# Kernel optimization log

Measured on AMD Instinct MI355X. Metric: run time of the kernel, lower is better.

Reference implementation:

```python
import jax, jax.numpy as jnp
import numpy as np

NUM_HEADS = 8
EMBED_CH = 512   # k channels
OUT_CH = 256     # v channels
MASK_CURRENT = False
NEG_INF = -1e30


def setup_inputs() -> dict:
    key = jax.random.key(0)
    ks = jax.random.split(key, 7)
    N, C, H, W = 8, 256, 32, 32
    s = lambda fan: 1.0 / np.sqrt(fan)
    return {
        "x": jax.random.normal(ks[0], (N, C, H, W), jnp.float32),
        "Wq": jax.random.normal(ks[1], (EMBED_CH, C), jnp.float32) * s(C),
        "bq": jax.random.normal(ks[2], (EMBED_CH,), jnp.float32) * 0.01,
        "Wkv": jax.random.normal(ks[3], (EMBED_CH + OUT_CH, C), jnp.float32) * s(C),
        "bkv": jax.random.normal(ks[4], (EMBED_CH + OUT_CH,), jnp.float32) * 0.01,
        "Wo": jax.random.normal(ks[5], (OUT_CH, OUT_CH), jnp.float32) * s(OUT_CH),
        "bo": jax.random.normal(ks[6], (OUT_CH,), jnp.float32) * 0.01,
    }


def _to_multihead(t, n, T):
    # t: [n, h*d, T] with channel layout '(h d)' -> [n, h, T, d]
    h = NUM_HEADS
    return t.reshape(n, h, -1, T).transpose(0, 1, 3, 2)


def reference(x, Wq, bq, Wkv, bkv, Wo, bo):
    n, C, H, W = x.shape
    T = H * W
    xf = x.reshape(n, C, T)  # flatten spatial dims into sequence

    # 1x1 convs == pointwise channel GEMMs
    q = jnp.einsum('oc,nct->not', Wq, xf) + bq[None, :, None]
    kv = jnp.einsum('oc,nct->not', Wkv, xf) + bkv[None, :, None]
    k, v = kv[:, :EMBED_CH], kv[:, EMBED_CH:]

    q = _to_multihead(q, n, T)   # [n, h, T, dk]
    k = _to_multihead(k, n, T)   # [n, h, T, dk]
    v = _to_multihead(v, n, T)   # [n, h, T, dv]

    dk = k.shape[-1]
    scale = 1.0 / np.sqrt(dk).astype(np.float32)

    # causal mask over flattened spatial positions (lower-triangular)
    diag = -1 if MASK_CURRENT else 0
    mask = jnp.tril(jnp.ones((T, T), dtype=bool), k=diag)  # [T, T]

    attn = jnp.einsum('nhtd,nhsd->nhts', q, k) * scale
    attn = jnp.where(mask[None, None], attn, NEG_INF)
    attn = jax.nn.softmax(attn, axis=-1)
    attn = jnp.where(mask[None, None], attn, 0.0)

    out = jnp.einsum('nhts,nhsd->nhtd', attn, v)            # [n, h, T, dv]
    out = out.transpose(0, 1, 3, 2).reshape(n, OUT_CH, T)   # n (h d) t

    out = jnp.einsum('oc,nct->not', Wo, out) + bo[None, :, None]
    return out.reshape(n, OUT_CH, H, W)
```

## Files before the change

kernel.cpp:

```cpp
#include <hip/hip_runtime.h>
#include <hip/hip_bf16.h>
#include <math.h>

typedef __bf16 bf16;
typedef __attribute__((ext_vector_type(4))) __bf16 bf16x4;
typedef __attribute__((ext_vector_type(8))) __bf16 bf16x8;
typedef __attribute__((ext_vector_type(4))) float f32x4;

#define T_DIM 1024
#define C_DIM 256
#define HEADS 8

static __device__ __forceinline__ int tb(int row, int col) {
  return row * 128 + ((((col >> 3) ^ row) & 7) << 4) + ((col & 7) << 1);
}

static __device__ __forceinline__ void gl16(const char* g, char* l) {
  __builtin_amdgcn_global_load_lds(
      (const __attribute__((address_space(1))) unsigned int*)g,
      (__attribute__((address_space(3))) unsigned int*)l, 16, 0, 0);
}
static __device__ __forceinline__ void stage16k(const char* g, char* l, int tid) {
  const int w = (tid >> 6) * 1024, ln = (tid & 63) * 16;
#pragma unroll
  for (int i = 0; i < 4; ++i) gl16(g + i * 4096 + w + ln, l + i * 4096 + w);
}
static __device__ __forceinline__ void stage8k(const char* g, char* l, int tid) {
  const int w = (tid >> 6) * 1024, ln = (tid & 63) * 16;
#pragma unroll
  for (int i = 0; i < 2; ++i) gl16(g + i * 4096 + w + ln, l + i * 4096 + w);
}
static __device__ __forceinline__ void stage4k(const char* g, char* l, int tid) {
  gl16(g + (tid >> 6) * 1024 + (tid & 63) * 16, l + (tid >> 6) * 1024);
}

__global__ __launch_bounds__(256) void k_prep(const float* __restrict__ x,
    const float* __restrict__ Wq, const float* __restrict__ Wkv, const float* __restrict__ Wo,
    char* __restrict__ xTt, char* __restrict__ Wbt, char* __restrict__ Wot) {
  const int tid = threadIdx.x;
  const int b = blockIdx.x;
  if (b < 512) {
    __shared__ float tile[64][65];
    const int n = b >> 6, rem = b & 63, tt64 = rem >> 2, ct = (rem & 3) << 6;
    const float* xp = x + ((size_t)n * C_DIM + ct) * T_DIM + tt64 * 64;
    const int t4 = (tid & 15) * 4, c0 = tid >> 4;
#pragma unroll
    for (int i = 0; i < 4; ++i) {
      const int c = c0 + i * 16;
      float4 v = *(const float4*)(xp + (size_t)c * T_DIM + t4);
      tile[c][t4] = v.x; tile[c][t4 + 1] = v.y; tile[c][t4 + 2] = v.z; tile[c][t4 + 3] = v.w;
    }
    __syncthreads();
    char* dst = xTt + (((size_t)(n * 8 + (tt64 >> 1))) * 4 + (rem & 3)) * 16384;
    const int rbase = (tt64 & 1) * 64;
#pragma unroll
    for (int i = 0; i < 2; ++i) {
      const int idx = tid + i * 256;
      const int tl = idx >> 3, c8 = (idx & 7) * 8;
      bf16x8 v;
#pragma unroll
      for (int j = 0; j < 8; ++j) v[j] = (bf16)tile[c8 + j][tl];
      *(bf16x8*)(dst + tb(rbase + tl, c8)) = v;
    }
  } else {
    const bool isWo = (b >= 532);
    const int o0 = (b - (isWo ? 532 : 512)) * 64;
#pragma unroll
    for (int i = 0; i < 8; ++i) {
      const int idx = tid + i * 256;
      const int row = idx >> 5, c8 = (idx & 31) * 8;
      const int o = o0 + row;
      const float* src = isWo ? (Wo + (size_t)o * C_DIM + c8)
                              : (o < 512 ? Wq + (size_t)o * C_DIM + c8
                                         : Wkv + (size_t)(o - 512) * C_DIM + c8);
      float4 a = *(const float4*)src;
      float4 bq4 = *(const float4*)(src + 4);
      bf16x8 v;
      v[0]=(bf16)a.x; v[1]=(bf16)a.y; v[2]=(bf16)a.z; v[3]=(bf16)a.w;
      v[4]=(bf16)bq4.x; v[5]=(bf16)bq4.y; v[6]=(bf16)bq4.z; v[7]=(bf16)bq4.w;
      char* base = isWo ? Wot : Wbt;
      char* dst = base + (((size_t)(o >> 7)) * 4 + (c8 >> 6)) * 16384;
      *(bf16x8*)(dst + tb(o & 127, c8 & 63)) = v;
    }
  }
}

__global__ __launch_bounds__(256) void k_qkv(const char* __restrict__ Wbt, const char* __restrict__ xTt,
    const float* __restrict__ bq, const float* __restrict__ bkv,
    bf16* __restrict__ q_ws, char* __restrict__ Kt, char* __restrict__ Vt) {
  __shared__ __attribute__((aligned(128))) unsigned char smem[34816];
  const int tid = threadIdx.x;
  const int nt = blockIdx.x, mt = blockIdx.y, n = blockIdx.z;
  const int w = tid >> 6, lane = tid & 63, lrow = lane & 15, lg = lane >> 4;
  const int wm = (w >> 1) * 64, wn = (w & 1) * 64;
  const char* gA = Wbt + (size_t)mt * 65536;
  const char* gB = xTt + ((size_t)(n * 8 + nt)) * 65536;
  const float s2 = 0.18033688f;

  f32x4 acc[4][4] = {};
#pragma unroll 1
  for (int kk = 0; kk < 4; ++kk) {
    stage16k(gA + kk * 16384, (char*)smem, tid);
    stage16k(gB + kk * 16384, (char*)smem + 16384, tid);
    __syncthreads();
    const char* As = (const char*)smem;
    const char* Bs = As + 16384;
    bf16x8 af[4][2], bv[4][2];
#pragma unroll
    for (int mi = 0; mi < 4; ++mi)
#pragma unroll
      for (int kh = 0; kh < 2; ++kh)
        af[mi][kh] = *(const bf16x8*)(As + tb(wm + mi * 16 + lrow, kh * 32 + lg * 8));
#pragma unroll
    for (int ni = 0; ni < 4; ++ni)
#pragma unroll
      for (int kh = 0; kh < 2; ++kh)
        bv[ni][kh] = *(const bf16x8*)(Bs + tb(wn + ni * 16 + lrow, kh * 32 + lg * 8));
#pragma unroll
    for (int kh = 0; kh < 2; ++kh)
#pragma unroll
      for (int mi = 0; mi < 4; ++mi)
#pragma unroll
        for (int ni = 0; ni < 4; ++ni)
          acc[mi][ni] = __builtin_amdgcn_mfma_f32_16x16x32_bf16(af[mi][kh], bv[ni][kh], acc[mi][ni], 0, 0, 0);
    __syncthreads();
  }

  const int obase = mt * 128 + wm + lg * 4;
  const int tcol0 = nt * 128 + wn + lrow;
  if (mt < 8) {
#pragma unroll
    for (int mi = 0; mi < 4; ++mi) {
      const int o = obase + mi * 16;
      if (mt < 4) {
        const float4 bb = *(const float4*)(bq + o);
        const int nh = n * 8 + (o >> 6), d = o & 63;
        bf16* qrow = q_ws + (size_t)nh * (T_DIM * 64) + d;
#pragma unroll
        for (int ni = 0; ni < 4; ++ni) {
          const int t = tcol0 + ni * 16;
          f32x4 v = acc[mi][ni];
          bf16x4 pk;
          pk[0]=(bf16)((v[0]+bb.x)*s2); pk[1]=(bf16)((v[1]+bb.y)*s2);
          pk[2]=(bf16)((v[2]+bb.z)*s2); pk[3]=(bf16)((v[3]+bb.w)*s2);
          *(bf16x4*)(qrow + (size_t)t * 64) = pk;
        }
      } else {
        const int o2 = o - 512;
        const float4 bb = *(const float4*)(bkv + o2);
        const int nh = n * 8 + (o2 >> 6), d = o2 & 63;
        char* tbase = Kt + (size_t)nh * 16 * 8192;
#pragma unroll
        for (int ni = 0; ni < 4; ++ni) {
          const int t = tcol0 + ni * 16;
          f32x4 v = acc[mi][ni];
          bf16x4 pk;
          pk[0]=(bf16)(v[0]+bb.x); pk[1]=(bf16)(v[1]+bb.y); pk[2]=(bf16)(v[2]+bb.z); pk[3]=(bf16)(v[3]+bb.w);
          *(bf16x4*)(tbase + (t >> 6) * 8192 + tb(t & 63, d)) = pk;
        }
      }
    }
  } else {
    bf16* tp = (bf16*)smem;
#pragma unroll
    for (int mi = 0; mi < 4; ++mi) {
      const int o3g = (mt - 8) * 128 + wm + mi * 16 + lg * 4;
      const float4 bb = *(const float4*)(bkv + 512 + o3g);
      const float* bbp = (const float*)&bb;
      const int o3l = wm + mi * 16 + lg * 4;
#pragma unroll
      for (int ni = 0; ni < 4; ++ni) {
        const int tl = wn + ni * 16 + lrow;
        f32x4 v = acc[mi][ni];
#pragma unroll
        for (int r = 0; r < 4; ++r)
          tp[(o3l + r) * 132 + tl] = (bf16)(v[r] + bbp[r]);
      }
    }
    __syncthreads();
    const int row = tid >> 1, half = tid & 1;
    const int o3 = (mt - 8) * 128 + row;
    const int nh = n * 8 + (o3 >> 5), dv = o3 & 31;
    char* tile = Vt + (size_t)nh * 16 * 4096 + (nt * 2 + half) * 4096;
    const bf16* src = tp + row * 132 + half * 64;
#pragma unroll
    for (int g = 0; g < 8; ++g) {
      bf16x4 lo = *(const bf16x4*)(src + g * 8);
      bf16x4 hi = *(const bf16x4*)(src + g * 8 + 4);
      bf16x8 vv;
      vv[0]=lo[0]; vv[1]=lo[1]; vv[2]=lo[2]; vv[3]=lo[3];
      vv[4]=hi[0]; vv[5]=hi[1]; vv[6]=hi[2]; vv[7]=hi[3];
      *(bf16x8*)(tile + tb(dv, g * 8)) = vv;
    }
  }
}

__global__ __launch_bounds__(256) void k_attn(const bf16* __restrict__ q_ws,
    const char* __restrict__ Kt, const char* __restrict__ Vt, char* __restrict__ attTt) {
  __shared__ __attribute__((aligned(128))) unsigned char smem[40960];
  const int tid = threadIdx.x;
  const int nh = blockIdx.x, qp = blockIdx.y;
  const int w = tid >> 6, lane = tid & 63, lrow = lane & 15, lg = lane >> 4;
  const int tl = w * 16 + lrow;
  const char* Ktb = Kt + (size_t)nh * 16 * 8192;
  const char* Vtb = Vt + (size_t)nh * 16 * 4096;
  const int n = nh >> 3, h = nh & 7;

  const int qt0 = qp, qt1 = 15 - qp;
  const int tg0 = qt0 * 64 + tl, tg1 = qt1 * 64 + tl;
  const bf16* qb0 = q_ws + ((size_t)nh * T_DIM + tg0) * 64;
  const bf16* qb1 = q_ws + ((size_t)nh * T_DIM + tg1) * 64;
  const bf16x8 qA0 = *(const bf16x8*)(qb0 + lg * 8);
  const bf16x8 qA1 = *(const bf16x8*)(qb0 + 32 + lg * 8);
  const bf16x8 qB0 = *(const bf16x8*)(qb1 + lg * 8);
  const bf16x8 qB1 = *(const bf16x8*)(qb1 + 32 + lg * 8);

  float l0 = 0.f, l1 = 0.f;
  f32x4 o0a = {}, o0b = {}, o1a = {}, o1b = {};

  auto proc = [&](bf16x8 qf0, bf16x8 qf1, float& l, f32x4& oa, f32x4& ob,
                  const char* Kbs, const char* Vbs, char* pws, bool diag) {
    f32x4 sacc[4];
    __builtin_amdgcn_s_setprio(1);
#pragma unroll
    for (int rt = 0; rt < 4; ++rt) {
      f32x4 a = {0.f, 0.f, 0.f, 0.f};
      bf16x8 kf0 = *(const bf16x8*)(Kbs + tb(rt * 16 + lrow, lg * 8));
      a = __builtin_amdgcn_mfma_f32_16x16x32_bf16(kf0, qf0, a, 0, 0, 0);
      bf16x8 kf1 = *(const bf16x8*)(Kbs + tb(rt * 16 + lrow, 32 + lg * 8));
      a = __builtin_amdgcn_mfma_f32_16x16x32_bf16(kf1, qf1, a, 0, 0, 0);
      sacc[rt] = a;
    }
    __builtin_amdgcn_s_setprio(0);
    float p[16];
#pragma unroll
    for (int rt = 0; rt < 4; ++rt)
#pragma unroll
      for (int r = 0; r < 4; ++r) {
        float e = __builtin_amdgcn_exp2f(sacc[rt][r]);
        if (diag && (rt * 16 + lg * 4 + r) > tl) e = 0.f;
        p[rt * 4 + r] = e;
      }
    float s0 = (p[0] + p[1]) + (p[2] + p[3]);
    float s1 = (p[4] + p[5]) + (p[6] + p[7]);
    float s2v = (p[8] + p[9]) + (p[10] + p[11]);
    float s3 = (p[12] + p[13]) + (p[14] + p[15]);
    float ps = (s0 + s1) + (s2v + s3);
    ps += __shfl_xor(ps, 16);
    ps += __shfl_xor(ps, 32);
    l += ps;
#pragma unroll
    for (int rt = 0; rt < 4; ++rt) {
      bf16x4 pk;
#pragma unroll
      for (int r = 0; r < 4; ++r) pk[r] = (bf16)p[rt * 4 + r];
      *(bf16x4*)(pws + tb(lrow, rt * 16 + lg * 4)) = pk;
    }
    __builtin_amdgcn_s_setprio(1);
#pragma unroll
    for (int ks = 0; ks < 2; ++ks) {
      bf16x8 pf = *(const bf16x8*)(pws + tb(lrow, ks * 32 + lg * 8));
      bf16x8 vf0 = *(const bf16x8*)(Vbs + tb(lrow, ks * 32 + lg * 8));
      oa = __builtin_amdgcn_mfma_f32_16x16x32_bf16(vf0, pf, oa, 0, 0, 0);
      bf16x8 vf1 = *(const bf16x8*)(Vbs + tb(16 + lrow, ks * 32 + lg * 8));
      ob = __builtin_amdgcn_mfma_f32_16x16x32_bf16(vf1, pf, ob, 0, 0, 0);
    }
    __builtin_amdgcn_s_setprio(0);
  };

#pragma unroll 1
  for (int st2 = 0; st2 <= qt1; st2 += 2) {
    const bool has1 = (st2 + 1 <= qt1);
    stage8k(Ktb + (size_t)st2 * 8192, (char*)smem, tid);
    if (has1) stage8k(Ktb + (size_t)(st2 + 1) * 8192, (char*)smem + 8192, tid);
    stage4k(Vtb + (size_t)st2 * 4096, (char*)smem + 16384, tid);
    if (has1) stage4k(Vtb + (size_t)(st2 + 1) * 4096, (char*)smem + 20480, tid);
    __syncthreads();
    const int nsub = has1 ? 2 : 1;
#pragma unroll 1
    for (int sub = 0; sub < nsub; ++sub) {
      const int stk = st2 + sub;
      const char* Kbs = (const char*)smem + sub * 8192;
      const char* Vbs = (const char*)smem + 16384 + sub * 4096;
      char* pws = (char*)smem + 24576 + w * 4096 + sub * 2048;
      proc(qB0, qB1, l1, o1a, o1b, Kbs, Vbs, pws, stk == qt1);
      if (stk <= qt0)
        proc(qA0, qA1, l0, o0a, o0b, Kbs, Vbs, pws, stk == qt0);
    }
    __syncthreads();
  }

  auto epi = [&](int tg, float l, f32x4 oa, f32x4 ob) {
    const float inv = 1.0f / l;
    const int ntt = tg >> 7, row = tg & 127;
#pragma unroll
    for (int dt = 0; dt < 2; ++dt) {
      const f32x4 v = dt ? ob : oa;
      const int c = h * 32 + dt * 16 + lg * 4;
      char* tile = attTt + (((size_t)(n * 8 + ntt)) * 4 + (c >> 6)) * 16384;
      bf16x4 pk;
#pragma unroll
      for (int r = 0; r < 4; ++r) pk[r] = (bf16)(v[r] * inv);
      *(bf16x4*)(tile + tb(row, c & 63)) = pk;
    }
  };
  epi(tg0, l0, o0a, o0b);
  epi(tg1, l1, o1a, o1b);
}

__global__ __launch_bounds__(256) void k_proj(const char* __restrict__ attTt,
    const char* __restrict__ Wot, const float* __restrict__ bo, float* __restrict__ out) {
  __shared__ __attribute__((aligned(128))) unsigned char smem[16384];
  const int tid = threadIdx.x;
  const int tm = blockIdx.x, om = blockIdx.y, n = blockIdx.z;
  const int w = tid >> 6, lane = tid & 63, lrow = lane & 15, lg = lane >> 4;
  const int wm = (w >> 1) * 32, wn = (w & 1) * 32;
  const char* gA = attTt + ((size_t)(n * 8 + (tm >> 1))) * 65536 + (tm & 1) * 8192;
  const char* gB = Wot + (size_t)(om >> 1) * 65536 + (om & 1) * 8192;

  f32x4 acc[2][2] = {};
#pragma unroll 1
  for (int kk = 0; kk < 4; ++kk) {
    stage8k(gA + kk * 16384, (char*)smem, tid);
    stage8k(gB + kk * 16384, (char*)smem + 8192, tid);
    __syncthreads();
    const char* As = (const char*)smem;
    const char* Bs = As + 8192;
    bf16x8 af[2][2], bv[2][2];
#pragma unroll
    for (int mi = 0; mi < 2; ++mi)
#pragma unroll
      for (int kh = 0; kh < 2; ++kh)
        af[mi][kh] = *(const bf16x8*)(As + tb(wm + mi * 16 + lrow, kh * 32 + lg * 8));
#pragma unroll
    for (int ni = 0; ni < 2; ++ni)
#pragma unroll
      for (int kh = 0; kh < 2; ++kh)
        bv[ni][kh] = *(const bf16x8*)(Bs + tb(wn + ni * 16 + lrow, kh * 32 + lg * 8));
#pragma unroll
    for (int kh = 0; kh < 2; ++kh)
#pragma unroll
      for (int mi = 0; mi < 2; ++mi)
#pragma unroll
        for (int ni = 0; ni < 2; ++ni)
          acc[mi][ni] = __builtin_amdgcn_mfma_f32_16x16x32_bf16(af[mi][kh], bv[ni][kh], acc[mi][ni], 0, 0, 0);
    __syncthreads();
  }

  const int t0b = tm * 64 + wm + lg * 4;
  const int ob = om * 64 + wn + lrow;
#pragma unroll
  for (int mi = 0; mi < 2; ++mi) {
    const int t0 = t0b + mi * 16;
#pragma unroll
    for (int ni = 0; ni < 2; ++ni) {
      const int o = ob + ni * 16;
      const float bb = bo[o];
      f32x4 v = acc[mi][ni];
      v[0] += bb; v[1] += bb; v[2] += bb; v[3] += bb;
      *(f32x4*)(out + ((size_t)(n * C_DIM + o)) * T_DIM + t0) = v;
    }
  }
}

extern "C" void kernel_launch(void* const* d_in, const int* in_sizes, int n_in,
                              void* d_out, int out_size, void* d_ws, size_t ws_size,
                              hipStream_t stream) {
  const float* x   = (const float*)d_in[0];
  const float* Wq  = (const float*)d_in[1];
  const float* bq  = (const float*)d_in[2];
  const float* Wkv = (const float*)d_in[3];
  const float* bkv = (const float*)d_in[4];
  const float* Wo  = (const float*)d_in[5];
  const float* bo  = (const float*)d_in[6];
  float* out = (float*)d_out;

  char* ws = (char*)d_ws;
  char* xTt   = ws;
  char* Wbt   = ws + (4u  << 20);
  char* Wot   = ws + (5u  << 20);
  bf16* q_ws  = (bf16*)(ws + (6u << 20));
  char* Kt    = ws + (14u << 20);
  char* Vt    = ws + (22u << 20);
  char* attTt = ws + (26u << 20);

  k_prep<<<536, 256, 0, stream>>>(x, Wq, Wkv, Wo, xTt, Wbt, Wot);
  k_qkv<<<dim3(8, 10, 8), 256, 0, stream>>>(Wbt, xTt, bq, bkv, q_ws, Kt, Vt);
  k_attn<<<dim3(64, 8), 256, 0, stream>>>(q_ws, Kt, Vt, attTt);
  k_proj<<<dim3(16, 4, 8), 256, 0, stream>>>(attTt, Wot, bo, out);
}
```

Baseline: 52.81 us.

## Replace direct-to-LDS loads with register-prefetched staging in all GEMM/attention kernels

The global_load_lds staging in the qkv, attention and projection kernels is replaced by loads into registers. Each next tile is issued right after the current tile is written to LDS, so the global fetch overlaps the MFMA work on the current tile. The trailing barrier in each loop is folded into the barrier at the top of the next iteration. In attention, the per-sub P scratch buffers are merged into one per wave, shrinking shared memory from 40KB to 32KB, which could allow more blocks per CU. Holding the prefetched data in registers adds pressure and may lower occupancy, and both sub-steps now share one P buffer.

After: 50.19 us, median of 2. -5.0%, faster.

```diff
diff --git a/kernel.cpp b/kernel.cpp
--- a/kernel.cpp
+++ b/kernel.cpp
@@ -13,25 +13,6 @@
 
 static __device__ __forceinline__ int tb(int row, int col) {
   return row * 128 + ((((col >> 3) ^ row) & 7) << 4) + ((col & 7) << 1);
-}
-
-static __device__ __forceinline__ void gl16(const char* g, char* l) {
-  __builtin_amdgcn_global_load_lds(
-      (const __attribute__((address_space(1))) unsigned int*)g,
-      (__attribute__((address_space(3))) unsigned int*)l, 16, 0, 0);
-}
-static __device__ __forceinline__ void stage16k(const char* g, char* l, int tid) {
-  const int w = (tid >> 6) * 1024, ln = (tid & 63) * 16;
-#pragma unroll
-  for (int i = 0; i < 4; ++i) gl16(g + i * 4096 + w + ln, l + i * 4096 + w);
-}
-static __device__ __forceinline__ void stage8k(const char* g, char* l, int tid) {
-  const int w = (tid >> 6) * 1024, ln = (tid & 63) * 16;
-#pragma unroll
-  for (int i = 0; i < 2; ++i) gl16(g + i * 4096 + w + ln, l + i * 4096 + w);
-}
-static __device__ __forceinline__ void stage4k(const char* g, char* l, int tid) {
-  gl16(g + (tid >> 6) * 1024 + (tid & 63) * 16, l + (tid >> 6) * 1024);
 }
 
 __global__ __launch_bounds__(256) void k_prep(const float* __restrict__ x,
@@ -96,12 +77,30 @@
   const char* gA = Wbt + (size_t)mt * 65536;
   const char* gB = xTt + ((size_t)(n * 8 + nt)) * 65536;
   const float s2 = 0.18033688f;
+  const int coff = w * 1024 + lane * 16;
+
+  bf16x8 sA0, sA1, sA2, sA3, sB0, sB1, sB2, sB3;
+  auto issue = [&](int kk) {
+    const char* a = gA + kk * 16384 + coff;
+    sA0 = *(const bf16x8*)(a);         sA1 = *(const bf16x8*)(a + 4096);
+    sA2 = *(const bf16x8*)(a + 8192);  sA3 = *(const bf16x8*)(a + 12288);
+    const char* bsrc = gB + kk * 16384 + coff;
+    sB0 = *(const bf16x8*)(bsrc);        sB1 = *(const bf16x8*)(bsrc + 4096);
+    sB2 = *(const bf16x8*)(bsrc + 8192); sB3 = *(const bf16x8*)(bsrc + 12288);
+  };
 
   f32x4 acc[4][4] = {};
+  issue(0);
 #pragma unroll 1
   for (int kk = 0; kk < 4; ++kk) {
-    stage16k(gA + kk * 16384, (char*)smem, tid);
-    stage16k(gB + kk * 16384, (char*)smem + 16384, tid);
+    __syncthreads();
+    char* da = (char*)smem + coff;
+    *(bf16x8*)(da)         = sA0; *(bf16x8*)(da + 4096)  = sA1;
+    *(bf16x8*)(da + 8192)  = sA2; *(bf16x8*)(da + 12288) = sA3;
+    char* db = (char*)smem + 16384 + coff;
+    *(bf16x8*)(db)         = sB0; *(bf16x8*)(db + 4096)  = sB1;
+    *(bf16x8*)(db + 8192)  = sB2; *(bf16x8*)(db + 12288) = sB3;
+    if (kk < 3) issue(kk + 1);
     __syncthreads();
     const char* As = (const char*)smem;
     const char* Bs = As + 16384;
@@ -123,8 +122,8 @@
 #pragma unroll
         for (int ni = 0; ni < 4; ++ni)
           acc[mi][ni] = __builtin_amdgcn_mfma_f32_16x16x32_bf16(af[mi][kh], bv[ni][kh], acc[mi][ni], 0, 0, 0);
-    __syncthreads();
-  }
+  }
+  __syncthreads();
 
   const int obase = mt * 128 + wm + lg * 4;
   const int tcol0 = nt * 128 + wn + lrow;
@@ -197,7 +196,7 @@
 
 __global__ __launch_bounds__(256) void k_attn(const bf16* __restrict__ q_ws,
     const char* __restrict__ Kt, const char* __restrict__ Vt, char* __restrict__ attTt) {
-  __shared__ __attribute__((aligned(128))) unsigned char smem[40960];
+  __shared__ __attribute__((aligned(128))) unsigned char smem[32768];
   const int tid = threadIdx.x;
   const int nh = blockIdx.x, qp = blockIdx.y;
   const int w = tid >> 6, lane = tid & 63, lrow = lane & 15, lg = lane >> 4;
@@ -205,6 +204,8 @@
   const char* Ktb = Kt + (size_t)nh * 16 * 8192;
   const char* Vtb = Vt + (size_t)nh * 16 * 4096;
   const int n = nh >> 3, h = nh & 7;
+  const int koff = w * 1024 + lane * 16;
+  const int voff = (tid >> 6) * 1024 + (tid & 63) * 16;
 
   const int qt0 = qp, qt1 = 15 - qp;
   const int tg0 = qt0 * 64 + tl, tg1 = qt1 * 64 + tl;
@@ -218,6 +219,20 @@
   float l0 = 0.f, l1 = 0.f;
   f32x4 o0a = {}, o0b = {}, o1a = {}, o1b = {};
 
+  bf16x8 s0, s1, s2, s3, s4, s5;
+  auto issue = [&](int st2, bool has1) {
+    const char* k0 = Ktb + (size_t)st2 * 8192 + koff;
+    s0 = *(const bf16x8*)(k0);
+    s1 = *(const bf16x8*)(k0 + 4096);
+    s4 = *(const bf16x8*)(Vtb + (size_t)st2 * 4096 + voff);
+    if (has1) {
+      const char* k1 = k0 + 8192;
+      s2 = *(const bf16x8*)(k1);
+      s3 = *(const bf16x8*)(k1 + 4096);
+      s5 = *(const bf16x8*)(Vtb + (size_t)(st2 + 1) * 4096 + voff);
+    }
+  };
+
   auto proc = [&](bf16x8 qf0, bf16x8 qf1, float& l, f32x4& oa, f32x4& ob,
                   const char* Kbs, const char* Vbs, char* pws, bool diag) {
     f32x4 sacc[4];
@@ -241,11 +256,11 @@
         if (diag && (rt * 16 + lg * 4 + r) > tl) e = 0.f;
         p[rt * 4 + r] = e;
       }
-    float s0 = (p[0] + p[1]) + (p[2] + p[3]);
-    float s1 = (p[4] + p[5]) + (p[6] + p[7]);
-    float s2v = (p[8] + p[9]) + (p[10] + p[11]);
-    float s3 = (p[12] + p[13]) + (p[14] + p[15]);
-    float ps = (s0 + s1) + (s2v + s3);
+    float t0 = (p[0] + p[1]) + (p[2] + p[3]);
+    float t1 = (p[4] + p[5]) + (p[6] + p[7]);
+    float t2 = (p[8] + p[9]) + (p[10] + p[11]);
+    float t3 = (p[12] + p[13]) + (p[14] + p[15]);
+    float ps = (t0 + t1) + (t2 + t3);
     ps += __shfl_xor(ps, 16);
     ps += __shfl_xor(ps, 32);
     l += ps;
@@ -268,13 +283,24 @@
     __builtin_amdgcn_s_setprio(0);
   };
 
+  issue(0, 1 <= qt1);
 #pragma unroll 1
   for (int st2 = 0; st2 <= qt1; st2 += 2) {
     const bool has1 = (st2 + 1 <= qt1);
-    stage8k(Ktb + (size_t)st2 * 8192, (char*)smem, tid);
-    if (has1) stage8k(Ktb + (size_t)(st2 + 1) * 8192, (char*)smem + 8192, tid);
-    stage4k(Vtb + (size_t)st2 * 4096, (char*)smem + 16384, tid);
-    if (has1) stage4k(Vtb + (size_t)(st2 + 1) * 4096, (char*)smem + 20480, tid);
+    __syncthreads();
+    {
+      char* kd = (char*)smem + koff;
+      *(bf16x8*)(kd) = s0;
+      *(bf16x8*)(kd + 4096) = s1;
+      *(bf16x8*)((char*)smem + 16384 + voff) = s4;
+      if (has1) {
+        *(bf16x8*)(kd + 8192) = s2;
+        *(bf16x8*)(kd + 12288) = s3;
+        *(bf16x8*)((char*)smem + 20480 + voff) = s5;
+      }
+    }
+    const int nst2 = st2 + 2;
+    if (nst2 <= qt1) issue(nst2, nst2 + 1 <= qt1);
     __syncthreads();
     const int nsub = has1 ? 2 : 1;
 #pragma unroll 1
@@ -282,12 +308,11 @@
       const int stk = st2 + sub;
       const char* Kbs = (const char*)smem + sub * 8192;
       const char* Vbs = (const char*)smem + 16384 + sub * 4096;
-      char* pws = (char*)smem + 24576 + w * 4096 + sub * 2048;
+      char* pws = (char*)smem + 24576 + w * 2048;
       proc(qB0, qB1, l1, o1a, o1b, Kbs, Vbs, pws, stk == qt1);
       if (stk <= qt0)
         proc(qA0, qA1, l0, o0a, o0b, Kbs, Vbs, pws, stk == qt0);
     }
-    __syncthreads();
   }
 
   auto epi = [&](int tg, float l, f32x4 oa, f32x4 ob) {
@@ -317,12 +342,26 @@
   const int wm = (w >> 1) * 32, wn = (w & 1) * 32;
   const char* gA = attTt + ((size_t)(n * 8 + (tm >> 1))) * 65536 + (tm & 1) * 8192;
   const char* gB = Wot + (size_t)(om >> 1) * 65536 + (om & 1) * 8192;
+  const int coff = w * 1024 + lane * 16;
+
+  bf16x8 pA0, pA1, pB0, pB1;
+  auto issue = [&](int kk) {
+    const char* a = gA + kk * 16384 + coff;
+    pA0 = *(const bf16x8*)(a); pA1 = *(const bf16x8*)(a + 4096);
+    const char* bsrc = gB + kk * 16384 + coff;
+    pB0 = *(const bf16x8*)(bsrc); pB1 = *(const bf16x8*)(bsrc + 4096);
+  };
 
   f32x4 acc[2][2] = {};
+  issue(0);
 #pragma unroll 1
   for (int kk = 0; kk < 4; ++kk) {
-    stage8k(gA + kk * 16384, (char*)smem, tid);
-    stage8k(gB + kk * 16384, (char*)smem + 8192, tid);
+    __syncthreads();
+    char* da = (char*)smem + coff;
+    *(bf16x8*)(da) = pA0; *(bf16x8*)(da + 4096) = pA1;
+    char* db = (char*)smem + 8192 + coff;
+    *(bf16x8*)(db) = pB0; *(bf16x8*)(db + 4096) = pB1;
+    if (kk < 3) issue(kk + 1);
     __syncthreads();
     const char* As = (const char*)smem;
     const char* Bs = As + 8192;
@@ -344,7 +383,6 @@
 #pragma unroll
         for (int ni = 0; ni < 2; ++ni)
           acc[mi][ni] = __builtin_amdgcn_mfma_f32_16x16x32_bf16(af[mi][kh], bv[ni][kh], acc[mi][ni], 0, 0, 0);
-    __syncthreads();
   }
 
   const int t0b = tm * 64 + wm + lg * 4;
```
